# Optimization experiments

Measured on AMD Instinct MI355X. Metric: run time of the kernel, lower is better.

Reference implementation:

```python
import jax, jax.numpy as jnp
import numpy as np

B, G, K, N, M, E, L = 8, 512, 64, 1024, 128, 4, 5

def _lin(x, w, b):
    return x @ w.T + b

def setup_inputs():
    key = jax.random.key(0)
    ks = jax.random.split(key, 20)
    def nrm(k, shape, s=1.0):
        return jax.random.normal(k, shape, dtype=jnp.float32) * s
    def lin_p(k, out_d, in_d):
        k1, k2 = jax.random.split(k)
        s = 1.0 / float(np.sqrt(in_d))
        return nrm(k1, (out_d, in_d), s), nrm(k2, (out_d,), s)
    inp = {}
    inp["z"] = nrm(ks[0], (B, G, K, M), 0.5)
    inp["hs_grid"] = nrm(ks[1], (B, G, M))
    inp["hs_key"] = nrm(ks[2], (B, K, M))
    inp["lig_rep"] = nrm(ks[3], (B, E))
    inp["hs_rec"] = nrm(ks[4], (B, N, M))
    inp["w_Rl"] = jnp.ones((1,), dtype=jnp.float32)
    inp["w_mask"] = jax.random.randint(ks[5], (B, K), 0, 2)
    dims = {"wra": (M, M), "wrh": (M, M), "wla": (M, M), "wlh": (M, M),
            "z1": (1, M), "wcR": (M, M), "wcl": (M, M), "kR": (M, M),
            "mapL": (L, 2 * M + E), "fin": (1, L)}
    for i, nm in enumerate(dims):
        w, b = lin_p(ks[6 + i], *dims[nm])
        inp[nm + "_w"] = w
        inp[nm + "_b"] = b
    return inp

def reference(z, hs_grid, hs_key, lig_rep, hs_rec, w_Rl, w_mask,
              wra_w, wra_b, wrh_w, wrh_b, wla_w, wla_b, wlh_w, wlh_b,
              z1_w, z1_b, wcR_w, wcR_b, wcl_w, wcl_b, kR_w, kR_b,
              mapL_w, mapL_b, fin_w, fin_b):
    exp_z = jnp.exp(z)                                    # [B,G,K,M]
    zr = exp_z / exp_z.sum(axis=-2, keepdims=True)        # pseudo-softmax over K
    ra = jnp.einsum('bgkm,bkm->bgm', zr, hs_key)          # [B,G,M]
    zl = exp_z / exp_z.sum(axis=-3, keepdims=True)        # pseudo-softmax over G
    la = jnp.einsum('bgkm,bgm->bkm', zl, hs_grid)         # [B,K,M]
    ra_rh = _lin(ra, wra_w, wra_b) + _lin(hs_grid, wrh_w, wrh_b)  # [B,G,M]
    la_lh = _lin(la, wla_w, wla_b) + _lin(hs_key, wlh_w, wlh_b)   # [B,K,M]
    att = _lin(z, z1_w, z1_b)[..., 0]                     # [B,G,K]
    att_l = jax.nn.softmax(att, axis=2).sum(axis=1)       # [B,K]
    att_r = jax.nn.softmax(att, axis=1).sum(axis=2)       # [B,G]
    key_rep = jnp.einsum('bk,bkm->bm', att_l, la_lh)      # [B,M]
    grid_rep = jnp.einsum('bg,bgm->bm', att_r, ra_rh)     # [B,M]
    Rh = _lin(hs_rec, wcR_w, wcR_b)                       # [B,N,M]
    lh = _lin(hs_key, wcl_w, wcl_b)                       # [B,K,M]
    z_Rl = jnp.einsum('bnh,bkh->bnk', Rh, lh)             # [B,N,K]
    masked = jnp.where(w_mask[:, None, :] == 0, jnp.float32(-1e10), w_Rl * z_Rl)
    z_Rl = jax.nn.softmax(masked, axis=1)                 # softmax over N
    kfr = jnp.einsum('bnk,bnh->bkh', z_Rl, hs_rec)        # [B,K,M]
    kfr = _lin(kfr, kR_w, kR_b)
    kfr = jnp.einsum('bk,bkh->bh', att_l, kfr)            # [B,M]
    key_rep = key_rep + kfr
    pair_rep = jnp.concatenate([key_rep, lig_rep, grid_rep], axis=1)  # [B,2M+E]
    pair_rep = _lin(pair_rep, mapL_w, mapL_b)             # [B,L]
    return _lin(pair_rep, fin_w, fin_b)[..., 0]           # [B]
```

## Files before the change

### kernel.cpp

```cpp
#include <hip/hip_runtime.h>

#define Bb 8
#define Gg 512
#define Kk 64
#define Nn 1024
#define Mm 128
#define KM 8192
#define GPB 16
#define NCH 32

struct K1Args {
  const float *z, *hs_grid, *hs_key, *z1w;
  const float *wra_w, *wrh_w, *wla_w, *wlh_w, *kR_w;
  const float *wla_b, *wlh_b, *kR_b, *wra_b, *wrh_b;
  const float *wcl_w, *wcl_b, *wcR_w;
  const float *mapL_w, *mapL_b, *fin_w, *fin_b;
  float *att, *laNum, *laDen, *ra, *Lk, *gbuf;
};

__global__ __launch_bounds__(1024) void K1(K1Args a) {
  __shared__ __align__(16) float smem[10240];
  const int bid = blockIdx.x;
  const int t = threadIdx.x;

  if (bid < 256) {
    float* s_hsgrid = smem;
    float* s_rn     = smem + 2048;
    float* s_rd     = smem + 6144;

    const int b = bid >> 5;
    const int gblk = bid & 31;
    const int lane_m = t & 31;
    const int m4 = lane_m << 2;
    const int kgrp = t >> 5;
    const int wv = t >> 6;

    const float* hgb = a.hs_grid + ((size_t)b * Gg + gblk * GPB) * Mm;
    for (int idx = t; idx < GPB * Mm; idx += 1024) s_hsgrid[idx] = hgb[idx];

    const int ofs0 = (kgrp * 2) * Mm + m4;
    const int ofs1 = ofs0 + Mm;
    const float4 hk0 = *reinterpret_cast<const float4*>(a.hs_key + (size_t)b * KM + ofs0);
    const float4 hk1 = *reinterpret_cast<const float4*>(a.hs_key + (size_t)b * KM + ofs1);

    const float zw0 = a.z1w[m4], zw1 = a.z1w[m4 + 1], zw2 = a.z1w[m4 + 2], zw3 = a.z1w[m4 + 3];

    float la_n[2][4], la_d[2][4];
#pragma unroll
    for (int i = 0; i < 2; ++i)
#pragma unroll
      for (int j = 0; j < 4; ++j) { la_n[i][j] = 0.f; la_d[i][j] = 0.f; }

    const float* zb = a.z + ((size_t)b * Gg + gblk * GPB) * (size_t)KM;
    float4 c0 = *reinterpret_cast<const float4*>(zb + ofs0);
    float4 c1 = *reinterpret_cast<const float4*>(zb + ofs1);

    __syncthreads();

    for (int gl = 0; gl < GPB; ++gl) {
      float4 n0 = c0, n1 = c1;
      if (gl < GPB - 1) {
        n0 = *reinterpret_cast<const float4*>(zb + (size_t)(gl + 1) * KM + ofs0);
        n1 = *reinterpret_cast<const float4*>(zb + (size_t)(gl + 1) * KM + ofs1);
      }
      const int g = gblk * GPB + gl;
      const float4 hg = *reinterpret_cast<const float4*>(s_hsgrid + gl * Mm + m4);
      float rn0 = 0, rn1 = 0, rn2 = 0, rn3 = 0, rd0 = 0, rd1 = 0, rd2 = 0, rd3 = 0;
#pragma unroll
      for (int i = 0; i < 2; ++i) {
        const float4 v = (i == 0) ? c0 : c1;
        const float4 hk = (i == 0) ? hk0 : hk1;
        const int k = kgrp * 2 + i;
        const float e0 = __expf(v.x), e1 = __expf(v.y), e2 = __expf(v.z), e3 = __expf(v.w);
        la_n[i][0] += e0 * hg.x; la_n[i][1] += e1 * hg.y; la_n[i][2] += e2 * hg.z; la_n[i][3] += e3 * hg.w;
        la_d[i][0] += e0;        la_d[i][1] += e1;        la_d[i][2] += e2;        la_d[i][3] += e3;
        rn0 += e0 * hk.x; rn1 += e1 * hk.y; rn2 += e2 * hk.z; rn3 += e3 * hk.w;
        rd0 += e0; rd1 += e1; rd2 += e2; rd3 += e3;
        float ap = v.x * zw0 + v.y * zw1 + v.z * zw2 + v.w * zw3;
        ap += __shfl_xor(ap, 16); ap += __shfl_xor(ap, 8); ap += __shfl_xor(ap, 4);
        ap += __shfl_xor(ap, 2);  ap += __shfl_xor(ap, 1);
        if (lane_m == 0) a.att[((size_t)b * Gg + g) * Kk + k] = ap;
      }
      rn0 += __shfl_xor(rn0, 32); rn1 += __shfl_xor(rn1, 32); rn2 += __shfl_xor(rn2, 32); rn3 += __shfl_xor(rn3, 32);
      rd0 += __shfl_xor(rd0, 32); rd1 += __shfl_xor(rd1, 32); rd2 += __shfl_xor(rd2, 32); rd3 += __shfl_xor(rd3, 32);
      float* rnB = s_rn + (gl & 1) * 2048;
      float* rdB = s_rd + (gl & 1) * 2048;
      if ((t & 63) < 32) {
        *reinterpret_cast<float4*>(rnB + wv * Mm + m4) = make_float4(rn0, rn1, rn2, rn3);
        *reinterpret_cast<float4*>(rdB + wv * Mm + m4) = make_float4(rd0, rd1, rd2, rd3);
      }
      __syncthreads();
      if (t < Mm) {
        float num = 0.f, den = 0.f;
#pragma unroll
        for (int ww = 0; ww < 16; ++ww) { num += rnB[ww * Mm + t]; den += rdB[ww * Mm + t]; }
        a.ra[((size_t)b * Gg + g) * Mm + t] = num / den;
      }
      c0 = n0; c1 = n1;
    }

    const size_t base = ((size_t)(b * NCH + gblk)) * KM;
#pragma unroll
    for (int i = 0; i < 2; ++i) {
      const int k = kgrp * 2 + i;
      *reinterpret_cast<float4*>(a.laNum + base + k * Mm + m4) =
          make_float4(la_n[i][0], la_n[i][1], la_n[i][2], la_n[i][3]);
      *reinterpret_cast<float4*>(a.laDen + base + k * Mm + m4) =
          make_float4(la_d[i][0], la_d[i][1], la_d[i][2], la_d[i][3]);
    }
  } else if (bid < 320) {
    float* s_w  = smem;
    float* s_lh = smem + 4224;
    const int blk = bid - 256;
    const int b = blk >> 3, k8 = blk & 7;
    const int m = t & 127, kq = t >> 7;
    const int k = k8 * 8 + kq;
    float lh = 0.f;
    for (int hc = 0; hc < 4; ++hc) {
      for (int i = t; i < 4096; i += 1024) {
        const int mm = i >> 5, hh = i & 31;
        s_w[hh * 132 + mm] = a.wcl_w[(size_t)mm * Mm + hc * 32 + hh];
      }
      __syncthreads();
      const float* keyb = a.hs_key + ((size_t)b * Kk + k) * Mm + hc * 32;
      for (int hh = 0; hh < 32; ++hh) lh += keyb[hh] * s_w[hh * 132 + m];
      __syncthreads();
    }
    s_lh[kq * 132 + m] = lh + a.wcl_b[m];
    __syncthreads();
    float acc = 0.f;
    for (int mm = 0; mm < 128; ++mm)
      acc += s_lh[kq * 132 + mm] * a.wcR_w[(size_t)mm * Mm + m];
    a.Lk[((size_t)b * Kk + k) * Mm + m] = acc;
  } else {
    float* s_fvec = smem;
    float* s_red  = smem + 260;
    if (t < 260) {
      float f = 0.f;
#pragma unroll
      for (int l = 0; l < 5; ++l) f += a.fin_w[l] * a.mapL_w[l * 260 + t];
      s_fvec[t] = f;
    }
    __syncthreads();
    const int h = t & 127, sel = t >> 7;
    if (sel < 5) {
      const float* W = (sel == 0) ? a.wla_w : (sel == 1) ? a.wlh_w :
                       (sel == 2) ? a.kR_w : (sel == 3) ? a.wra_w : a.wrh_w;
      const float* fv = (sel < 3) ? s_fvec : (s_fvec + 132);
      float g = 0.f;
      for (int mm = 0; mm < 128; ++mm) g += fv[mm] * W[(size_t)mm * Mm + h];
      a.gbuf[sel * 128 + h] = g;
    }
    if (t < 128) {
      s_red[t] = s_fvec[t] * (a.wla_b[t] + a.wlh_b[t] + a.kR_b[t]);
      s_red[128 + t] = s_fvec[132 + t] * (a.wra_b[t] + a.wrh_b[t]);
    }
    __syncthreads();
    if (t == 0) {
      float c1 = 0.f, c2 = 0.f;
      for (int i = 0; i < 128; ++i) { c1 += s_red[i]; c2 += s_red[128 + i]; }
      float C = a.fin_b[0];
#pragma unroll
      for (int l = 0; l < 5; ++l) C += a.fin_w[l] * a.mapL_b[l];
      a.gbuf[640] = C + 512.0f * c1 + 64.0f * c2;
#pragma unroll
      for (int e = 0; e < 4; ++e) a.gbuf[641 + e] = s_fvec[128 + e];
    }
  }
}

struct K2Args {
  const float *laNum, *laDen, *hs_key, *att, *ra, *hs_grid, *Lk, *hs_rec;
  const int *mask;
  const float *wRl, *gbuf;
  float *attlP, *attrPM, *attrPS, *attrPR, *pmT, *psT, *PSpT, *laDot, *keyDot;
};

__global__ __launch_bounds__(256) void K2(K2Args a) {
  __shared__ __align__(16) float smem[4944];
  const int bid = blockIdx.x;
  const int t = threadIdx.x;

  if (bid < 64) {
    const int b = bid >> 3, k8 = bid & 7;
    const int m = t & 127, kh = t >> 7;
    const float g1 = a.gbuf[m], g2 = a.gbuf[128 + m];
    float* sl = smem;
    float* sk = smem + 1056;
#pragma unroll
    for (int i = 0; i < 4; ++i) {
      const int k = k8 * 8 + kh * 4 + i;
      const float* np = a.laNum + (size_t)b * NCH * KM + (size_t)k * Mm + m;
      const float* dp = a.laDen + (size_t)b * NCH * KM + (size_t)k * Mm + m;
      float num = 0.f, den = 0.f;
#pragma unroll 8
      for (int p = 0; p < NCH; ++p) { num += np[(size_t)p * KM]; den += dp[(size_t)p * KM]; }
      sl[(kh * 4 + i) * 132 + m] = g1 * (num / den);
      sk[(kh * 4 + i) * 132 + m] = g2 * a.hs_key[((size_t)b * Kk + k) * Mm + m];
    }
    __syncthreads();
    const int rid = t >> 5, l32 = t & 31;
    float s1 = sl[rid * 132 + l32] + sl[rid * 132 + l32 + 32] +
               sl[rid * 132 + l32 + 64] + sl[rid * 132 + l32 + 96];
    float s2 = sk[rid * 132 + l32] + sk[rid * 132 + l32 + 32] +
               sk[rid * 132 + l32 + 64] + sk[rid * 132 + l32 + 96];
#pragma unroll
    for (int off = 16; off; off >>= 1) { s1 += __shfl_xor(s1, off); s2 += __shfl_xor(s2, off); }
    if (l32 == 0) {
      a.laDot[b * Kk + k8 * 8 + rid] = s1;
      a.keyDot[b * Kk + k8 * 8 + rid] = s2;
    }
  } else if (bid < 128) {
    const int blk = bid - 64;
    const int b = blk >> 3, p = blk & 7;
    const int w = t >> 6, lane = t & 63;
    float acc = 0.f;
    for (int j = 0; j < 16; ++j) {
      const int g = p * 64 + w * 16 + j;
      const float av = a.att[((size_t)b * Gg + g) * Kk + lane];
      float mx = av;
      for (int off = 32; off; off >>= 1) mx = fmaxf(mx, __shfl_xor(mx, off));
      const float e = __expf(av - mx);
      float s = e;
      for (int off = 32; off; off >>= 1) s += __shfl_xor(s, off);
      acc += e / s;
    }
    float* sred = smem;
    sred[w * 64 + lane] = acc;
    __syncthreads();
    if (t < 64) a.attlP[(b * 8 + p) * 64 + t] = sred[t] + sred[64 + t] + sred[128 + t] + sred[192 + t];
  } else if (bid < 192) {
    const int blk = bid - 128;
    const int b = blk >> 3, gc = blk & 7;
    float* s_gw   = smem;
    float* s_rdot = smem + 256;
    float* sm = smem + 320;
    float* ss = smem + 576;
    float* sr = smem + 832;
    s_gw[t] = a.gbuf[384 + t];
    __syncthreads();
    {
      const int gg = t >> 2, q = t & 3;
      const int g = gc * 64 + gg;
      const float* rp_ = a.ra + ((size_t)b * Gg + g) * Mm + q * 32;
      const float* hp = a.hs_grid + ((size_t)b * Gg + g) * Mm + q * 32;
      float acc = 0.f;
#pragma unroll
      for (int j4 = 0; j4 < 8; ++j4) {
        const float4 rv = *reinterpret_cast<const float4*>(rp_ + j4 * 4);
        const float4 hv = *reinterpret_cast<const float4*>(hp + j4 * 4);
        const int mb = q * 32 + j4 * 4;
        acc += s_gw[mb + 0] * rv.x + s_gw[128 + mb + 0] * hv.x;
        acc += s_gw[mb + 1] * rv.y + s_gw[128 + mb + 1] * hv.y;
        acc += s_gw[mb + 2] * rv.z + s_gw[128 + mb + 2] * hv.z;
        acc += s_gw[mb + 3] * rv.w + s_gw[128 + mb + 3] * hv.w;
      }
      acc += __shfl_xor(acc, 1);
      acc += __shfl_xor(acc, 2);
      if (q == 0) s_rdot[gg] = acc;
    }
    __syncthreads();
    const int k = t & 63, j4 = t >> 6;
    float m_ = -3.0e38f, s_ = 0.f, r_ = 0.f;
    for (int j = 0; j < 16; ++j) {
      const int gg = j4 * 16 + j;
      const float av = a.att[((size_t)b * Gg + gc * 64 + gg) * Kk + k];
      const float rv = s_rdot[gg];
      if (av > m_) {
        const float sc = __expf(m_ - av);
        s_ = s_ * sc + 1.0f; r_ = r_ * sc + rv; m_ = av;
      } else {
        const float e = __expf(av - m_);
        s_ += e; r_ += e * rv;
      }
    }
    sm[j4 * 64 + k] = m_; ss[j4 * 64 + k] = s_; sr[j4 * 64 + k] = r_;
    __syncthreads();
    if (t < 64) {
      float M = sm[t];
      for (int q = 1; q < 4; ++q) M = fmaxf(M, sm[q * 64 + t]);
      float S = 0.f, R = 0.f;
      for (int q = 0; q < 4; ++q) {
        const float e = __expf(sm[q * 64 + t] - M);
        S += ss[q * 64 + t] * e; R += sr[q * 64 + t] * e;
      }
      const int o = (b * 8 + gc) * 64 + t;
      a.attrPM[o] = M; a.attrPS[o] = S; a.attrPR[o] = R;
    }
  } else {
    const int vb = bid - 192;
    const int b = vb >> 6, ntile = vb & 63;
    const int n0 = ntile * 16;
    const int k = t & 63;
    const int hq = __builtin_amdgcn_readfirstlane(t >> 6);
    float* s_acc = smem;
    float* s_m   = smem + 4096;
    float* s_s   = smem + 4352;
    float* s_p   = smem + 4608;
    float* s_ru4 = smem + 4864;
    float* s_ru  = smem + 4928;
    float rLk[32];
    {
      const float* Lp = a.Lk + ((size_t)b * Kk + k) * Mm + hq * 32;
#pragma unroll
      for (int j = 0; j < 8; ++j) {
        const float4 v = *reinterpret_cast<const float4*>(Lp + j * 4);
        rLk[j * 4 + 0] = v.x; rLk[j * 4 + 1] = v.y;
        rLk[j * 4 + 2] = v.z; rLk[j * 4 + 3] = v.w;
      }
    }
    float acc[16];
    const float* rb = a.hs_rec + ((size_t)b * Nn + n0) * Mm + hq * 32;
#pragma unroll
    for (int r = 0; r < 16; ++r) {
      const float* rp = rb + r * Mm;
      float s = 0.f;
#pragma unroll
      for (int j4 = 0; j4 < 8; ++j4) {
        const float4 rv = *reinterpret_cast<const float4*>(rp + j4 * 4);
        s += rv.x * rLk[j4 * 4] + rv.y * rLk[j4 * 4 + 1] +
             rv.z * rLk[j4 * 4 + 2] + rv.w * rLk[j4 * 4 + 3];
      }
      acc[r] = s;
    }
#pragma unroll
    for (int r = 0; r < 16; ++r) s_acc[(hq * 16 + r) * 64 + k] = acc[r];
    if (t < 64) {
      const int rt = t >> 2, hc = t & 3;
      const float* rp = a.hs_rec + ((size_t)b * Nn + n0 + rt) * Mm + hc * 32;
      const float* gu = a.gbuf + 256 + hc * 32;
      float s = 0.f;
#pragma unroll
      for (int j = 0; j < 32; ++j) s += gu[j] * rp[j];
      s_ru4[rt * 4 + hc] = s;
    }
    __syncthreads();
    if (t < 16) s_ru[t] = s_ru4[t * 4] + s_ru4[t * 4 + 1] + s_ru4[t * 4 + 2] + s_ru4[t * 4 + 3];
    __syncthreads();
    const float wv = a.wRl[0];
    const bool msk = (a.mask[b * Kk + k] == 0);
    float m = -3.0e38f, ssum = 0.f, psum = 0.f;
    const int hq4 = (t >> 6) * 4;
#pragma unroll
    for (int q = 0; q < 4; ++q) {
      const int r = hq4 + q;
      float v = s_acc[r * 64 + k] + s_acc[(16 + r) * 64 + k] +
                s_acc[(32 + r) * 64 + k] + s_acc[(48 + r) * 64 + k];
      v = msk ? -1e10f : wv * v;
      const float runow = s_ru[r];
      if (v > m) {
        const float sc = __expf(m - v);
        ssum = ssum * sc + 1.0f; psum = psum * sc + runow; m = v;
      } else {
        const float e = __expf(v - m);
        ssum += e; psum += e * runow;
      }
    }
    s_m[(t >> 6) * 64 + k] = m; s_s[(t >> 6) * 64 + k] = ssum; s_p[(t >> 6) * 64 + k] = psum;
    __syncthreads();
    if (t < 64) {
      float M = fmaxf(fmaxf(s_m[t], s_m[64 + t]), fmaxf(s_m[128 + t], s_m[192 + t]));
      float S = 0.f, P = 0.f;
#pragma unroll
      for (int q = 0; q < 4; ++q) {
        const float e = __expf(s_m[q * 64 + t] - M);
        S += s_s[q * 64 + t] * e; P += s_p[q * 64 + t] * e;
      }
      const size_t o = ((size_t)b * 64 + ntile) * 64 + t;
      a.pmT[o] = M; a.psT[o] = S; a.PSpT[o] = P;
    }
  }
}

__global__ __launch_bounds__(64) void K3(
    const float* __restrict__ attlP, const float* __restrict__ pmT,
    const float* __restrict__ psT, const float* __restrict__ PSpT,
    const float* __restrict__ attrPM, const float* __restrict__ attrPS,
    const float* __restrict__ attrPR,
    const float* __restrict__ laDot, const float* __restrict__ keyDot,
    const float* __restrict__ gbuf, const float* __restrict__ lig_rep,
    float* __restrict__ out)
{
  const int b = blockIdx.x, t = threadIdx.x;
  float attl = 0.f;
#pragma unroll
  for (int p = 0; p < 8; ++p) attl += attlP[(b * 8 + p) * 64 + t];
  float M = -3.0e38f, S = 0.f, P = 0.f;
  for (int nt = 0; nt < 64; ++nt) {
    const size_t o = ((size_t)b * 64 + nt) * 64 + t;
    const float pm_ = pmT[o], ps_ = psT[o], pp = PSpT[o];
    if (pm_ > M) {
      const float sc = __expf(M - pm_);
      S = S * sc + ps_; P = P * sc + pp; M = pm_;
    } else {
      const float e = __expf(pm_ - M);
      S += ps_ * e; P += pp * e;
    }
  }
  float Mr = -3.0e38f, Sr = 0.f, Rr = 0.f;
  for (int p = 0; p < 8; ++p) {
    const int o = (b * 8 + p) * 64 + t;
    const float pm_ = attrPM[o], ps_ = attrPS[o], pr_ = attrPR[o];
    if (pm_ > Mr) {
      const float sc = __expf(Mr - pm_);
      Sr = Sr * sc + ps_; Rr = Rr * sc + pr_; Mr = pm_;
    } else {
      const float e = __expf(pm_ - Mr);
      Sr += ps_ * e; Rr += pr_ * e;
    }
  }
  float val = attl * (laDot[b * 64 + t] + keyDot[b * 64 + t] + P / S) + Rr / Sr;
#pragma unroll
  for (int off = 32; off; off >>= 1) val += __shfl_xor(val, off);
  if (t == 0) {
    float o = val + gbuf[640];
#pragma unroll
    for (int e = 0; e < 4; ++e) o += gbuf[641 + e] * lig_rep[b * 4 + e];
    out[b] = o;
  }
}

extern "C" void kernel_launch(void* const* d_in, const int* in_sizes, int n_in,
                              void* d_out, int out_size, void* d_ws, size_t ws_size,
                              hipStream_t stream) {
  float* w = (float*)d_ws;
  float* gbuf  = w;
  float* att   = gbuf + 1024;
  float* laNum = att + Bb * Gg * Kk;
  float* laDen = laNum + Bb * NCH * KM;
  float* ra    = laDen + Bb * NCH * KM;
  float* Lk    = ra + Bb * Gg * Mm;
  float* attlP = Lk + Bb * Kk * Mm;
  float* pmT   = attlP + Bb * 8 * 64;
  float* psT   = pmT + Bb * 64 * 64;
  float* PSpT  = psT + Bb * 64 * 64;
  float* laDot = PSpT + Bb * 64 * 64;
  float* keyDot = laDot + Bb * Kk;
  float* attrPM = keyDot + Bb * Kk;
  float* attrPS = attrPM + Bb * 8 * 64;
  float* attrPR = attrPS + Bb * 8 * 64;

  K1Args a1;
  a1.z = (const float*)d_in[0];
  a1.hs_grid = (const float*)d_in[1];
  a1.hs_key = (const float*)d_in[2];
  a1.z1w = (const float*)d_in[15];
  a1.wra_w = (const float*)d_in[7];  a1.wra_b = (const float*)d_in[8];
  a1.wrh_w = (const float*)d_in[9];  a1.wrh_b = (const float*)d_in[10];
  a1.wla_w = (const float*)d_in[11]; a1.wla_b = (const float*)d_in[12];
  a1.wlh_w = (const float*)d_in[13]; a1.wlh_b = (const float*)d_in[14];
  a1.wcl_w = (const float*)d_in[19]; a1.wcl_b = (const float*)d_in[20];
  a1.wcR_w = (const float*)d_in[17];
  a1.kR_w  = (const float*)d_in[21]; a1.kR_b = (const float*)d_in[22];
  a1.mapL_w = (const float*)d_in[23]; a1.mapL_b = (const float*)d_in[24];
  a1.fin_w = (const float*)d_in[25]; a1.fin_b = (const float*)d_in[26];
  a1.att = att; a1.laNum = laNum; a1.laDen = laDen;
  a1.ra = ra; a1.Lk = Lk; a1.gbuf = gbuf;

  K2Args a2;
  a2.laNum = laNum; a2.laDen = laDen;
  a2.hs_key = (const float*)d_in[2];
  a2.att = att; a2.ra = ra;
  a2.hs_grid = (const float*)d_in[1];
  a2.Lk = Lk;
  a2.hs_rec = (const float*)d_in[4];
  a2.mask = (const int*)d_in[6];
  a2.wRl = (const float*)d_in[5];
  a2.gbuf = gbuf;
  a2.attlP = attlP;
  a2.attrPM = attrPM; a2.attrPS = attrPS; a2.attrPR = attrPR;
  a2.pmT = pmT; a2.psT = psT; a2.PSpT = PSpT;
  a2.laDot = laDot; a2.keyDot = keyDot;

  K1<<<321, 1024, 0, stream>>>(a1);
  K2<<<704, 256, 0, stream>>>(a2);
  K3<<<Bb, 64, 0, stream>>>(attlP, pmT, psT, PSpT, attrPM, attrPS, attrPR,
                            laDot, keyDot, gbuf, (const float*)d_in[3],
                            (float*)d_out);
}
```

Baseline: 105.3 us.

## Split ra reduction over K into separate blocks, removing per-g block barriers

The ra computation (softmax over K weighted by hs_key) moves out of the main z-streaming blocks into 128 new blocks, each handling 32 grid positions with one warp per g and reducing over K in registers. This removes the per-g cross-warp shared-memory reduction and its __syncthreads from the main loop and shrinks shared memory. The cost is that z is read from global memory a second time (another full pass over the 16M-element tensor) and exp is computed twice.

```diff
diff --git a/kernel.cpp b/kernel.cpp
--- a/kernel.cpp
+++ b/kernel.cpp
@@ -19,30 +19,23 @@
 };
 
 __global__ __launch_bounds__(1024) void K1(K1Args a) {
-  __shared__ __align__(16) float smem[10240];
+  __shared__ __align__(16) float smem[8192];
   const int bid = blockIdx.x;
   const int t = threadIdx.x;
 
   if (bid < 256) {
     float* s_hsgrid = smem;
-    float* s_rn     = smem + 2048;
-    float* s_rd     = smem + 6144;
-
     const int b = bid >> 5;
     const int gblk = bid & 31;
     const int lane_m = t & 31;
     const int m4 = lane_m << 2;
     const int kgrp = t >> 5;
-    const int wv = t >> 6;
 
     const float* hgb = a.hs_grid + ((size_t)b * Gg + gblk * GPB) * Mm;
     for (int idx = t; idx < GPB * Mm; idx += 1024) s_hsgrid[idx] = hgb[idx];
 
     const int ofs0 = (kgrp * 2) * Mm + m4;
     const int ofs1 = ofs0 + Mm;
-    const float4 hk0 = *reinterpret_cast<const float4*>(a.hs_key + (size_t)b * KM + ofs0);
-    const float4 hk1 = *reinterpret_cast<const float4*>(a.hs_key + (size_t)b * KM + ofs1);
-
     const float zw0 = a.z1w[m4], zw1 = a.z1w[m4 + 1], zw2 = a.z1w[m4 + 2], zw3 = a.z1w[m4 + 3];
 
     float la_n[2][4], la_d[2][4];
@@ -65,36 +58,17 @@
       }
       const int g = gblk * GPB + gl;
       const float4 hg = *reinterpret_cast<const float4*>(s_hsgrid + gl * Mm + m4);
-      float rn0 = 0, rn1 = 0, rn2 = 0, rn3 = 0, rd0 = 0, rd1 = 0, rd2 = 0, rd3 = 0;
 #pragma unroll
       for (int i = 0; i < 2; ++i) {
         const float4 v = (i == 0) ? c0 : c1;
-        const float4 hk = (i == 0) ? hk0 : hk1;
         const int k = kgrp * 2 + i;
         const float e0 = __expf(v.x), e1 = __expf(v.y), e2 = __expf(v.z), e3 = __expf(v.w);
         la_n[i][0] += e0 * hg.x; la_n[i][1] += e1 * hg.y; la_n[i][2] += e2 * hg.z; la_n[i][3] += e3 * hg.w;
         la_d[i][0] += e0;        la_d[i][1] += e1;        la_d[i][2] += e2;        la_d[i][3] += e3;
-        rn0 += e0 * hk.x; rn1 += e1 * hk.y; rn2 += e2 * hk.z; rn3 += e3 * hk.w;
-        rd0 += e0; rd1 += e1; rd2 += e2; rd3 += e3;
         float ap = v.x * zw0 + v.y * zw1 + v.z * zw2 + v.w * zw3;
         ap += __shfl_xor(ap, 16); ap += __shfl_xor(ap, 8); ap += __shfl_xor(ap, 4);
         ap += __shfl_xor(ap, 2);  ap += __shfl_xor(ap, 1);
         if (lane_m == 0) a.att[((size_t)b * Gg + g) * Kk + k] = ap;
-      }
-      rn0 += __shfl_xor(rn0, 32); rn1 += __shfl_xor(rn1, 32); rn2 += __shfl_xor(rn2, 32); rn3 += __shfl_xor(rn3, 32);
-      rd0 += __shfl_xor(rd0, 32); rd1 += __shfl_xor(rd1, 32); rd2 += __shfl_xor(rd2, 32); rd3 += __shfl_xor(rd3, 32);
-      float* rnB = s_rn + (gl & 1) * 2048;
-      float* rdB = s_rd + (gl & 1) * 2048;
-      if ((t & 63) < 32) {
-        *reinterpret_cast<float4*>(rnB + wv * Mm + m4) = make_float4(rn0, rn1, rn2, rn3);
-        *reinterpret_cast<float4*>(rdB + wv * Mm + m4) = make_float4(rd0, rd1, rd2, rd3);
-      }
-      __syncthreads();
-      if (t < Mm) {
-        float num = 0.f, den = 0.f;
-#pragma unroll
-        for (int ww = 0; ww < 16; ++ww) { num += rnB[ww * Mm + t]; den += rdB[ww * Mm + t]; }
-        a.ra[((size_t)b * Gg + g) * Mm + t] = num / den;
       }
       c0 = n0; c1 = n1;
     }
@@ -108,10 +82,36 @@
       *reinterpret_cast<float4*>(a.laDen + base + k * Mm + m4) =
           make_float4(la_d[i][0], la_d[i][1], la_d[i][2], la_d[i][3]);
     }
-  } else if (bid < 320) {
+  } else if (bid < 384) {
+    float* s_hskey = smem;
+    const int blk = bid - 256;
+    const int b = blk >> 4;
+    const int gch = blk & 15;
+    const int gslot = t >> 5;
+    const int m4 = (t & 31) << 2;
+    const int g = gch * 32 + gslot;
+
+    const float* hkb = a.hs_key + (size_t)b * KM;
+    for (int idx = t; idx < KM; idx += 1024) s_hskey[idx] = hkb[idx];
+    __syncthreads();
+
+    const float* zg = a.z + ((size_t)b * Gg + g) * (size_t)KM + m4;
+    float n0 = 0.f, n1 = 0.f, n2 = 0.f, n3 = 0.f;
+    float d0 = 0.f, d1 = 0.f, d2 = 0.f, d3 = 0.f;
+#pragma unroll 4
+    for (int k = 0; k < Kk; ++k) {
+      const float4 v = *reinterpret_cast<const float4*>(zg + (size_t)k * Mm);
+      const float4 hk = *reinterpret_cast<const float4*>(s_hskey + k * Mm + m4);
+      const float e0 = __expf(v.x), e1 = __expf(v.y), e2 = __expf(v.z), e3 = __expf(v.w);
+      n0 += e0 * hk.x; n1 += e1 * hk.y; n2 += e2 * hk.z; n3 += e3 * hk.w;
+      d0 += e0; d1 += e1; d2 += e2; d3 += e3;
+    }
+    *reinterpret_cast<float4*>(a.ra + ((size_t)b * Gg + g) * Mm + m4) =
+        make_float4(n0 / d0, n1 / d1, n2 / d2, n3 / d3);
+  } else if (bid < 448) {
     float* s_w  = smem;
     float* s_lh = smem + 4224;
-    const int blk = bid - 256;
+    const int blk = bid - 384;
     const int b = blk >> 3, k8 = blk & 7;
     const int m = t & 127, kq = t >> 7;
     const int k = k8 * 8 + kq;
@@ -472,7 +472,7 @@
   a2.pmT = pmT; a2.psT = psT; a2.PSpT = PSpT;
   a2.laDot = laDot; a2.keyDot = keyDot;
 
-  K1<<<321, 1024, 0, stream>>>(a1);
+  K1<<<449, 1024, 0, stream>>>(a1);
   K2<<<704, 256, 0, stream>>>(a2);
   K3<<<Bb, 64, 0, stream>>>(attlP, pmT, psT, PSpT, attrPM, attrPS, attrPR,
                             laDot, keyDot, gbuf, (const float*)d_in[3],
```

Result: slower. 147.4 us (+39.9%).
